# Kernel optimization log

Measured on AMD Instinct MI355X. Metric: run time of the kernel, lower is better.

The kernel has to match this reference:

```python
import jax, jax.numpy as jnp
import numpy as np

N_NODES = 50000
N_EDGES = 800000
N_FEAT = 512
N_HID = 256
N_LAYER = 4
N_CLASS = 40


def setup_inputs() -> dict:
    key = jax.random.key(0)
    ks = jax.random.split(key, 16)
    x = jax.random.normal(ks[0], (N_NODES, N_FEAT), dtype=jnp.float32)
    edge_index = jax.random.randint(ks[1], (2, N_EDGES), 0, N_NODES, dtype=jnp.int64 if jax.config.jax_enable_x64 else jnp.int32)

    def glorot(k, fan_in, fan_out):
        lim = np.sqrt(6.0 / (fan_in + fan_out)).astype(np.float32)
        return jax.random.uniform(k, (fan_in, fan_out), jnp.float32, -lim, lim)

    in_gc_W = glorot(ks[2], N_FEAT, N_HID)
    in_gc_b = jnp.zeros((N_HID,), jnp.float32)
    in_lin_W = glorot(ks[3], N_FEAT, N_HID)
    in_lin_b = jnp.zeros((N_HID,), jnp.float32)
    # n_layer-1 = 3 hidden conv / lin pairs, stacked on leading axis
    convs_W = jnp.stack([glorot(jax.random.fold_in(ks[4], i), N_HID, N_HID) for i in range(N_LAYER - 1)])
    convs_b = jnp.zeros((N_LAYER - 1, N_HID), jnp.float32)
    lins_W = jnp.stack([glorot(jax.random.fold_in(ks[5], i), N_HID, N_HID) for i in range(N_LAYER - 1)])
    lins_b = jnp.zeros((N_LAYER - 1, N_HID), jnp.float32)
    out_W = glorot(ks[6], N_HID * N_LAYER, N_CLASS)
    out_b = jnp.zeros((N_CLASS,), jnp.float32)
    return {
        "x": x, "edge_index": edge_index,
        "in_gc_W": in_gc_W, "in_gc_b": in_gc_b,
        "in_lin_W": in_lin_W, "in_lin_b": in_lin_b,
        "convs_W": convs_W, "convs_b": convs_b,
        "lins_W": lins_W, "lins_b": lins_b,
        "out_W": out_W, "out_b": out_b,
    }


def reference(x, edge_index, in_gc_W, in_gc_b, in_lin_W, in_lin_b,
              convs_W, convs_b, lins_W, lins_b, out_W, out_b):
    src, dst = edge_index[0], edge_index[1]
    n = x.shape[0]
    # GCN symmetric normalization with self-loops: deg = 1 + in-degree
    deg = jnp.zeros((n,), jnp.float32).at[dst].add(1.0) + 1.0
    dinv = jax.lax.rsqrt(deg)
    edge_norm = dinv[src] * dinv[dst]        # [E]
    self_norm = dinv * dinv                  # [N]

    def gcn(h, W, b):
        hw = h @ W                           # [N, out]
        msg = hw[src] * edge_norm[:, None]   # gather + scale
        agg = jax.ops.segment_sum(msg, dst, num_segments=n)
        agg = agg + hw * self_norm[:, None]  # self-loop term
        return agg + b

    # inductive: GCNConv + linear residual; dropout = identity (eval mode)
    h = jax.nn.relu(gcn(x, in_gc_W, in_gc_b) + x @ in_lin_W + in_lin_b)
    xs = [h]
    for i in range(convs_W.shape[0]):
        h = jax.nn.relu(gcn(h, convs_W[i], convs_b[i]) + h @ lins_W[i] + lins_b[i])
        xs.append(h)
    # JumpingKnowledge mode='cat'
    jk = jnp.concatenate(xs, axis=-1)        # [N, n_hid * n_layer]
    return jk @ out_W + out_b
```

## Files before the change

kernel.cpp:

```cpp
#include <hip/hip_runtime.h>

typedef _Float16 half8 __attribute__((ext_vector_type(8)));
typedef _Float16 half4 __attribute__((ext_vector_type(4)));
typedef float floatx4 __attribute__((ext_vector_type(4)));

__device__ __forceinline__ void gld16(const _Float16* g, _Float16* lds_base) {
    __builtin_amdgcn_global_load_lds(
        (const __attribute__((address_space(1))) unsigned int*)g,
        (__attribute__((address_space(3))) unsigned int*)lds_base,
        16, 0, 0);
}

__global__ __launch_bounds__(256) void zero_i32(int* __restrict__ p, int n) {
    int i = blockIdx.x * 256 + threadIdx.x;
    if (i < n) p[i] = 0;
}

__global__ __launch_bounds__(256) void hist_dst(const int* __restrict__ dst,
                                                int* __restrict__ count, int E) {
    int e = blockIdx.x * 256 + threadIdx.x;
    if (e < E) atomicAdd(&count[dst[e]], 1);
}

__global__ __launch_bounds__(256) void cast_f32_f16(const float* __restrict__ in,
                                                    _Float16* __restrict__ out, int n4) {
    int i = blockIdx.x * 256 + threadIdx.x;
    if (i < n4) {
        float4 v = *(const float4*)&in[(size_t)i * 4];
        half4 h = { (_Float16)v.x, (_Float16)v.y, (_Float16)v.z, (_Float16)v.w };
        *(half4*)&out[(size_t)i * 4] = h;
    }
}

__global__ __launch_bounds__(256) void transpose_cast_tiled(
    const float* __restrict__ W, _Float16* __restrict__ WT, int K, int N)
{
    __shared__ _Float16 t[32][33];
    const int k0 = blockIdx.x * 32, n0 = blockIdx.y * 32;
    const int tx = threadIdx.x & 31, ty = threadIdx.x >> 5;
    #pragma unroll
    for (int i = 0; i < 4; ++i) {
        int k = k0 + ty + i * 8, n = n0 + tx;
        float v = (k < K && n < N) ? W[(size_t)k * N + n] : 0.0f;
        t[ty + i * 8][tx] = (_Float16)v;
    }
    __syncthreads();
    #pragma unroll
    for (int i = 0; i < 4; ++i) {
        int n = n0 + ty + i * 8, k = k0 + tx;
        if (n < N && k < K) WT[(size_t)n * K + k] = t[tx][ty + i * 8];
    }
}

__global__ __launch_bounds__(256) void scan_block(const int* __restrict__ count,
                                                  int* __restrict__ incl,
                                                  int* __restrict__ blocksum,
                                                  float* __restrict__ dinv, int n) {
    __shared__ int tmp[256];
    int t = threadIdx.x;
    int i = blockIdx.x * 256 + t;
    int v = (i < n) ? count[i] : 0;
    if (i < n) dinv[i] = rsqrtf(1.0f + (float)v);
    tmp[t] = v;
    __syncthreads();
    for (int off = 1; off < 256; off <<= 1) {
        int x = (t >= off) ? tmp[t - off] : 0;
        __syncthreads();
        tmp[t] += x;
        __syncthreads();
    }
    if (i < n) incl[i] = tmp[t];
    if (t == 255) blocksum[blockIdx.x] = tmp[255];
}

__global__ __launch_bounds__(256) void scan_top(const int* __restrict__ blocksum,
                                                int* __restrict__ blockoff, int nb) {
    __shared__ int tmp[256];
    int t = threadIdx.x;
    int v = (t < nb) ? blocksum[t] : 0;
    tmp[t] = v;
    __syncthreads();
    for (int off = 1; off < 256; off <<= 1) {
        int x = (t >= off) ? tmp[t - off] : 0;
        __syncthreads();
        tmp[t] += x;
        __syncthreads();
    }
    if (t < nb) blockoff[t] = tmp[t] - v;
}

__global__ __launch_bounds__(256) void make_rowptr(const int* __restrict__ incl,
                                                   const int* __restrict__ count,
                                                   const int* __restrict__ blockoff,
                                                   int* __restrict__ rowptr,
                                                   int* __restrict__ cursor, int n) {
    int i = blockIdx.x * 256 + threadIdx.x;
    if (i < n) {
        int r = incl[i] - count[i] + blockoff[blockIdx.x];
        rowptr[i] = r;
        cursor[i] = r;
    }
}

__global__ __launch_bounds__(256) void scatter_perm(const int* __restrict__ src,
                                                    const int* __restrict__ dst,
                                                    const float* __restrict__ dinv,
                                                    int* __restrict__ cursor,
                                                    int2* __restrict__ sorted_meta, int E) {
    int e = blockIdx.x * 256 + threadIdx.x;
    if (e < E) {
        int d = dst[e], s = src[e];
        int slot = atomicAdd(&cursor[d], 1);
        sorted_meta[slot] = make_int2(s, __float_as_int(dinv[s] * dinv[d]));
    }
}

template<bool DUAL>
__global__ __launch_bounds__(256) void gemm_mfma(
    const _Float16* __restrict__ A, int lda,
    const _Float16* __restrict__ BT, int Nrows,
    const float* __restrict__ bias0, const float* __restrict__ bias1,
    _Float16* __restrict__ lin_h, _Float16* __restrict__ hw,
    float* __restrict__ Cf, int ldc,
    int M, int K)
{
    __shared__ _Float16 As[128 * 64];
    __shared__ _Float16 Bs[128 * 64];

    const int tid  = threadIdx.x;
    const int wave = tid >> 6;
    const int lane = tid & 63;
    const int q    = lane >> 4;
    const int r    = lane & 15;

    const int wm = (wave & 1) * 64;
    const int wn = (wave >> 1) * 64;

    const int bn = blockIdx.x * 128;
    const int bm = blockIdx.y * 128;

    const int srow  = wave * 32;
    const int lrow8 = lane >> 3;
    const int cp    = lane & 7;

    floatx4 acc[4][4] = {};

    for (int k0 = 0; k0 < K; k0 += 64) {
        #pragma unroll
        for (int t = 0; t < 4; ++t) {
            int lrow = srow + t * 8 + lrow8;
            int c    = cp ^ (lrow & 7);
            int gm = bm + lrow; if (gm > M - 1) gm = M - 1;
            gld16(&A[(size_t)gm * lda + k0 + c * 8], &As[(srow + t * 8) * 64]);
            int gn = bn + lrow; if (gn > Nrows - 1) gn = Nrows - 1;
            gld16(&BT[(size_t)gn * K + k0 + c * 8], &Bs[(srow + t * 8) * 64]);
        }
        __syncthreads();

        #pragma unroll
        for (int kk = 0; kk < 2; ++kk) {
            const int sc = ((kk << 2) | q) ^ (r & 7);
            half8 af[4], bf[4];
            #pragma unroll
            for (int mi = 0; mi < 4; ++mi)
                af[mi] = *(const half8*)&As[(wm + mi * 16 + r) * 64 + sc * 8];
            #pragma unroll
            for (int ni = 0; ni < 4; ++ni)
                bf[ni] = *(const half8*)&Bs[(wn + ni * 16 + r) * 64 + sc * 8];
            #pragma unroll
            for (int mi = 0; mi < 4; ++mi)
                #pragma unroll
                for (int ni = 0; ni < 4; ++ni)
                    acc[mi][ni] = __builtin_amdgcn_mfma_f32_16x16x32_f16(
                        af[mi], bf[ni], acc[mi][ni], 0, 0, 0);
        }
        __syncthreads();
    }

    if (DUAL) {
        const bool islin = (bn < 256);
        _Float16* dstp = islin ? lin_h : hw;
        #pragma unroll
        for (int ni = 0; ni < 4; ++ni) {
            int col = bn + wn + ni * 16 + r;
            int c2  = islin ? col : col - 256;
            float badd = islin ? (bias0[col] + bias1[col]) : 0.0f;
            #pragma unroll
            for (int mi = 0; mi < 4; ++mi)
                #pragma unroll
                for (int reg = 0; reg < 4; ++reg) {
                    int gm = bm + wm + mi * 16 + q * 4 + reg;
                    if (gm < M)
                        dstp[(size_t)gm * 256 + c2] = (_Float16)(acc[mi][ni][reg] + badd);
                }
        }
    } else {
        #pragma unroll
        for (int ni = 0; ni < 4; ++ni) {
            int col = bn + wn + ni * 16 + r;
            if (col >= Nrows) continue;
            float badd = bias0 ? bias0[col] : 0.0f;
            #pragma unroll
            for (int mi = 0; mi < 4; ++mi)
                #pragma unroll
                for (int reg = 0; reg < 4; ++reg) {
                    int gm = bm + wm + mi * 16 + q * 4 + reg;
                    if (gm < M)
                        Cf[(size_t)gm * ldc + col] = acc[mi][ni][reg] + badd;
                }
        }
    }
}

__global__ __launch_bounds__(256) void aggregate_csr(
    const int* __restrict__ rowptr, const int* __restrict__ count,
    const int2* __restrict__ sorted_meta,
    const float* __restrict__ dinv,
    const _Float16* __restrict__ hw,
    const _Float16* __restrict__ lin_h,
    _Float16* __restrict__ jk_col, int n)
{
    const int bx    = blockIdx.x;
    const int xslot = bx & 7;
    const int half  = xslot >> 2;
    const int chunk = ((bx >> 3) << 2) + (xslot & 3);
    const int wave  = threadIdx.x >> 6;
    const int lane  = threadIdx.x & 63;
    const int i     = chunk * 4 + wave;
    if (i >= n) return;

    const int qw = lane >> 4;
    const int fl = lane & 15;
    const int fbase = half * 128 + fl * 8;

    const int start = rowptr[i];
    const int deg   = count[i];

    float accf[8] = {};
    if (qw == 0) {
        half8 l8 = *(const half8*)&lin_h[(size_t)i * 256 + fbase];
        #pragma unroll
        for (int t = 0; t < 8; ++t) accf[t] = (float)l8[t];
    } else if (qw == 1) {
        float di = dinv[i];
        float sn = di * di;
        half8 s8 = *(const half8*)&hw[(size_t)i * 256 + fbase];
        #pragma unroll
        for (int t = 0; t < 8; ++t) accf[t] = (float)s8[t] * sn;
    }

    for (int base = 0; base < deg; base += 64) {
        int m = deg - base;
        if (m > 64) m = 64;
        int2 meta = make_int2(0, 0);
        if (lane < m) meta = sorted_meta[start + base + lane];

        for (int j = 0; j < m; j += 16) {
            half8 hv[4];
            float nm[4];
            #pragma unroll
            for (int k2 = 0; k2 < 4; ++k2) {
                int e   = j + k2 * 4 + qw;
                int idx = (e < m) ? e : (m - 1);
                int s   = __shfl(meta.x, idx, 64);
                int nmb = __shfl(meta.y, idx, 64);
                nm[k2]  = (e < m) ? __int_as_float(nmb) : 0.0f;
                hv[k2]  = *(const half8*)&hw[(size_t)s * 256 + fbase];
            }
            #pragma unroll
            for (int k2 = 0; k2 < 4; ++k2)
                #pragma unroll
                for (int t = 0; t < 8; ++t)
                    accf[t] = fmaf((float)hv[k2][t], nm[k2], accf[t]);
        }
    }

    #pragma unroll
    for (int t = 0; t < 8; ++t) {
        accf[t] += __shfl_xor(accf[t], 16, 64);
        accf[t] += __shfl_xor(accf[t], 32, 64);
    }

    if (qw == 0) {
        half8 o;
        #pragma unroll
        for (int t = 0; t < 8; ++t) o[t] = (_Float16)fmaxf(accf[t], 0.0f);
        *(half8*)&jk_col[(size_t)i * 1024 + fbase] = o;
    }
}

extern "C" void kernel_launch(void* const* d_in, const int* in_sizes, int n_in,
                              void* d_out, int out_size, void* d_ws, size_t ws_size,
                              hipStream_t stream) {
    const float* x        = (const float*)d_in[0];
    const int*   ei       = (const int*)d_in[1];
    const float* in_gc_W  = (const float*)d_in[2];
    const float* in_gc_b  = (const float*)d_in[3];
    const float* in_lin_W = (const float*)d_in[4];
    const float* in_lin_b = (const float*)d_in[5];
    const float* convs_W  = (const float*)d_in[6];
    const float* convs_b  = (const float*)d_in[7];
    const float* lins_W   = (const float*)d_in[8];
    const float* lins_b   = (const float*)d_in[9];
    const float* out_W    = (const float*)d_in[10];
    const float* out_b    = (const float*)d_in[11];

    const int N = 50000;
    const int E = in_sizes[1] / 2;
    const int F = 512, H = 256, L = 4, NC = 40;

    const int* src = ei;
    const int* dst = ei + E;

    char* ws = (char*)d_ws;
    auto carve = [&](size_t bytes) { void* p = ws; ws += (bytes + 255) & ~(size_t)255; return p; };
    float*    dinv        = (float*)carve((size_t)N * 4);
    int*      count       = (int*)  carve((size_t)N * 4);
    int*      incl        = (int*)  carve((size_t)N * 4);
    int*      rowptr      = (int*)  carve((size_t)N * 4);
    int*      cursor      = (int*)  carve((size_t)N * 4);
    int*      blocksum    = (int*)  carve(256 * 4);
    int*      blockoff    = (int*)  carve(256 * 4);
    int2*     sorted_meta = (int2*) carve((size_t)E * 8);
    _Float16* xh          = (_Float16*)carve((size_t)N * F * 2);
    _Float16* w0comb      = (_Float16*)carve((size_t)512 * F * 2);
    _Float16* wcomb       = (_Float16*)carve((size_t)3 * 512 * H * 2);
    _Float16* outWT       = (_Float16*)carve((size_t)NC * H * L * 2);
    _Float16* lin_h       = (_Float16*)carve((size_t)N * H * 2);
    _Float16* hw          = (_Float16*)carve((size_t)N * H * 2);
    _Float16* jk_h        = (_Float16*)carve((size_t)N * H * L * 2);
    float*    out         = (float*)d_out;

    const int nbN = (N + 255) / 256;
    const int nbE = (E + 255) / 256;

    zero_i32<<<nbN, 256, 0, stream>>>(count, N);
    hist_dst<<<nbE, 256, 0, stream>>>(dst, count, E);
    scan_block<<<nbN, 256, 0, stream>>>(count, incl, blocksum, dinv, N);
    scan_top<<<1, 256, 0, stream>>>(blocksum, blockoff, nbN);
    make_rowptr<<<nbN, 256, 0, stream>>>(incl, count, blockoff, rowptr, cursor, N);
    scatter_perm<<<nbE, 256, 0, stream>>>(src, dst, dinv, cursor, sorted_meta, E);

    cast_f32_f16<<<(N * F / 4 + 255) / 256, 256, 0, stream>>>(x, xh, N * F / 4);
    {
        dim3 tg((F + 31) / 32, (H + 31) / 32);
        transpose_cast_tiled<<<tg, 256, 0, stream>>>(in_lin_W, w0comb,                F, H);
        transpose_cast_tiled<<<tg, 256, 0, stream>>>(in_gc_W,  w0comb + (size_t)H * F, F, H);
        dim3 th((H + 31) / 32, (H + 31) / 32);
        for (int l = 0; l < 3; ++l) {
            _Float16* wl = wcomb + (size_t)l * 512 * H;
            transpose_cast_tiled<<<th, 256, 0, stream>>>(lins_W  + (size_t)l * H * H, wl,                 H, H);
            transpose_cast_tiled<<<th, 256, 0, stream>>>(convs_W + (size_t)l * H * H, wl + (size_t)H * H, H, H);
        }
        dim3 to((H * L + 31) / 32, (NC + 31) / 32);
        transpose_cast_tiled<<<to, 256, 0, stream>>>(out_W, outWT, H * L, NC);
    }

    const dim3 dgrid(4, (N + 127) / 128);
    const dim3 ogrid(1, (N + 127) / 128);
    const int agg_blocks = 2 * ((N + 3) / 4);

    for (int l = 0; l < L; ++l) {
        const _Float16* Ah = (l == 0) ? xh : (jk_h + (size_t)(l - 1) * H);
        int lda            = (l == 0) ? F : H * L;
        int K              = (l == 0) ? F : H;
        const _Float16* BT = (l == 0) ? w0comb : (wcomb + (size_t)(l - 1) * 512 * H);
        const float* gcB   = (l == 0) ? in_gc_b  : (convs_b + (size_t)(l - 1) * H);
        const float* liB   = (l == 0) ? in_lin_b : (lins_b  + (size_t)(l - 1) * H);

        gemm_mfma<true><<<dgrid, 256, 0, stream>>>(Ah, lda, BT, 512, liB, gcB,
                                                   lin_h, hw, nullptr, 0, N, K);
        aggregate_csr<<<agg_blocks, 256, 0, stream>>>(rowptr, count, sorted_meta,
                                                      dinv, hw, lin_h, jk_h + (size_t)l * H, N);
    }

    gemm_mfma<false><<<ogrid, 256, 0, stream>>>(jk_h, H * L, outWT, NC, out_b, nullptr,
                                                nullptr, nullptr, out, NC, N, H * L);
}
```

Baseline: 725.8 us.

## Fuse setup kernels, remap GEMM grid for XCD locality, specialize output GEMM, simplify aggregation

Folds the count zeroing into a wider 8-element fp32-to-fp16 cast kernel and collapses the eight weight transpose launches into three batched launches. The dual GEMM now uses a 1D grid with a block-index swizzle that groups M tiles across XCD slots. The output projection gets a dedicated 256-row kernel that uses a 64-wide N tile instead of 128. The CSR aggregation drops the shuffle-based metadata broadcast in favour of direct per-lane metadata loads, eight edges deep. Together these cut launch count and wasted output-GEMM work, but the metadata reads are now redundant across lanes and the swizzle may shift L2 behaviour.

Measured after the change: 816.9 us. +12.6%, slower.

```diff
diff --git a/kernel.cpp b/kernel.cpp
--- a/kernel.cpp
+++ b/kernel.cpp
@@ -11,9 +11,18 @@
         16, 0, 0);
 }
 
-__global__ __launch_bounds__(256) void zero_i32(int* __restrict__ p, int n) {
+__global__ __launch_bounds__(256) void cast_x_zero(const float* __restrict__ in,
+                                                   _Float16* __restrict__ out, int n8,
+                                                   int* __restrict__ count, int nzero) {
     int i = blockIdx.x * 256 + threadIdx.x;
-    if (i < n) p[i] = 0;
+    if (i < n8) {
+        float4 v0 = *(const float4*)&in[(size_t)i * 8];
+        float4 v1 = *(const float4*)&in[(size_t)i * 8 + 4];
+        half8 h = { (_Float16)v0.x, (_Float16)v0.y, (_Float16)v0.z, (_Float16)v0.w,
+                    (_Float16)v1.x, (_Float16)v1.y, (_Float16)v1.z, (_Float16)v1.w };
+        *(half8*)&out[(size_t)i * 8] = h;
+    }
+    if (i < nzero) count[i] = 0;
 }
 
 __global__ __launch_bounds__(256) void hist_dst(const int* __restrict__ dst,
@@ -22,22 +31,9 @@
     if (e < E) atomicAdd(&count[dst[e]], 1);
 }
 
-__global__ __launch_bounds__(256) void cast_f32_f16(const float* __restrict__ in,
-                                                    _Float16* __restrict__ out, int n4) {
-    int i = blockIdx.x * 256 + threadIdx.x;
-    if (i < n4) {
-        float4 v = *(const float4*)&in[(size_t)i * 4];
-        half4 h = { (_Float16)v.x, (_Float16)v.y, (_Float16)v.z, (_Float16)v.w };
-        *(half4*)&out[(size_t)i * 4] = h;
-    }
-}
-
-__global__ __launch_bounds__(256) void transpose_cast_tiled(
-    const float* __restrict__ W, _Float16* __restrict__ WT, int K, int N)
-{
+__device__ __forceinline__ void tc_tile(const float* W, _Float16* WT, int K, int N,
+                                        int k0, int n0, int tx, int ty) {
     __shared__ _Float16 t[32][33];
-    const int k0 = blockIdx.x * 32, n0 = blockIdx.y * 32;
-    const int tx = threadIdx.x & 31, ty = threadIdx.x >> 5;
     #pragma unroll
     for (int i = 0; i < 4; ++i) {
         int k = k0 + ty + i * 8, n = n0 + tx;
@@ -50,6 +46,34 @@
         int n = n0 + ty + i * 8, k = k0 + tx;
         if (n < N && k < K) WT[(size_t)n * K + k] = t[tx][ty + i * 8];
     }
+}
+
+__global__ __launch_bounds__(256) void transpose_cast_in(
+    const float* __restrict__ Wl, const float* __restrict__ Wg,
+    _Float16* __restrict__ dst, int K, int N)
+{
+    const float* W = blockIdx.z ? Wg : Wl;
+    _Float16* D = dst + (size_t)blockIdx.z * N * K;
+    tc_tile(W, D, K, N, blockIdx.x * 32, blockIdx.y * 32,
+            threadIdx.x & 31, threadIdx.x >> 5);
+}
+
+__global__ __launch_bounds__(256) void transpose_cast_hid(
+    const float* __restrict__ lins, const float* __restrict__ convs,
+    _Float16* __restrict__ wcomb)
+{
+    const int l = blockIdx.z >> 1, j = blockIdx.z & 1;
+    const float* W = (j ? convs : lins) + (size_t)l * 256 * 256;
+    _Float16* D = wcomb + (size_t)l * 512 * 256 + (size_t)j * 256 * 256;
+    tc_tile(W, D, 256, 256, blockIdx.x * 32, blockIdx.y * 32,
+            threadIdx.x & 31, threadIdx.x >> 5);
+}
+
+__global__ __launch_bounds__(256) void transpose_cast_one(
+    const float* __restrict__ W, _Float16* __restrict__ WT, int K, int N)
+{
+    tc_tile(W, WT, K, N, blockIdx.x * 32, blockIdx.y * 32,
+            threadIdx.x & 31, threadIdx.x >> 5);
 }
 
 __global__ __launch_bounds__(256) void scan_block(const int* __restrict__ count,
@@ -115,33 +139,28 @@
     }
 }
 
-template<bool DUAL>
-__global__ __launch_bounds__(256) void gemm_mfma(
+__global__ __launch_bounds__(256) void gemm_dual(
     const _Float16* __restrict__ A, int lda,
-    const _Float16* __restrict__ BT, int Nrows,
+    const _Float16* __restrict__ BT, int K,
     const float* __restrict__ bias0, const float* __restrict__ bias1,
     _Float16* __restrict__ lin_h, _Float16* __restrict__ hw,
-    float* __restrict__ Cf, int ldc,
-    int M, int K)
-{
+    int M, int m_tiles)
+{
+    const int b     = blockIdx.x;
+    const int x     = b & 7;
+    const int inner = b >> 3;
+    const int n_t   = inner & 3;
+    const int m_t   = (inner >> 2) * 8 + x;
+    if (m_t >= m_tiles) return;
+    const int bm = m_t * 128, bn = n_t * 128;
+
     __shared__ _Float16 As[128 * 64];
     __shared__ _Float16 Bs[128 * 64];
 
-    const int tid  = threadIdx.x;
-    const int wave = tid >> 6;
-    const int lane = tid & 63;
-    const int q    = lane >> 4;
-    const int r    = lane & 15;
-
-    const int wm = (wave & 1) * 64;
-    const int wn = (wave >> 1) * 64;
-
-    const int bn = blockIdx.x * 128;
-    const int bm = blockIdx.y * 128;
-
-    const int srow  = wave * 32;
-    const int lrow8 = lane >> 3;
-    const int cp    = lane & 7;
+    const int wave = threadIdx.x >> 6, lane = threadIdx.x & 63;
+    const int q = lane >> 4, r = lane & 15;
+    const int wm = (wave & 1) * 64, wn = (wave >> 1) * 64;
+    const int srow = wave * 32, lrow8 = lane >> 3, cp = lane & 7;
 
     floatx4 acc[4][4] = {};
 
@@ -152,7 +171,7 @@
             int c    = cp ^ (lrow & 7);
             int gm = bm + lrow; if (gm > M - 1) gm = M - 1;
             gld16(&A[(size_t)gm * lda + k0 + c * 8], &As[(srow + t * 8) * 64]);
-            int gn = bn + lrow; if (gn > Nrows - 1) gn = Nrows - 1;
+            int gn = bn + lrow;
             gld16(&BT[(size_t)gn * K + k0 + c * 8], &Bs[(srow + t * 8) * 64]);
         }
         __syncthreads();
@@ -177,39 +196,101 @@
         __syncthreads();
     }
 
-    if (DUAL) {
-        const bool islin = (bn < 256);
-        _Float16* dstp = islin ? lin_h : hw;
-        #pragma unroll
-        for (int ni = 0; ni < 4; ++ni) {
-            int col = bn + wn + ni * 16 + r;
-            int c2  = islin ? col : col - 256;
-            float badd = islin ? (bias0[col] + bias1[col]) : 0.0f;
+    const bool islin = (bn < 256);
+    _Float16* dstp = islin ? lin_h : hw;
+    const int cbase = (islin ? bn : bn - 256) + wn;
+    float badd[4];
+    #pragma unroll
+    for (int ni = 0; ni < 4; ++ni) {
+        int col = bn + wn + ni * 16 + r;
+        badd[ni] = islin ? (bias0[col] + bias1[col]) : 0.0f;
+    }
+    #pragma unroll
+    for (int mi = 0; mi < 4; ++mi)
+        #pragma unroll
+        for (int reg = 0; reg < 4; ++reg) {
+            int gm = bm + wm + mi * 16 + q * 4 + reg;
+            if (gm >= M) continue;
+            #pragma unroll
+            for (int ni = 0; ni < 4; ++ni)
+                dstp[(size_t)gm * 256 + cbase + ni * 16 + r] =
+                    (_Float16)(acc[mi][ni][reg] + badd[ni]);
+        }
+}
+
+__global__ __launch_bounds__(256) void gemm_out(
+    const _Float16* __restrict__ A,
+    const _Float16* __restrict__ BT,
+    const float* __restrict__ bias,
+    float* __restrict__ Cf, int M)
+{
+    const int bm = blockIdx.x * 256;
+    __shared__ _Float16 As[256 * 64];
+    __shared__ _Float16 Bs[64 * 64];
+
+    const int wave = threadIdx.x >> 6, lane = threadIdx.x & 63;
+    const int q = lane >> 4, r = lane & 15;
+    const int wm = wave * 64;
+    const int lrow8 = lane >> 3, cp = lane & 7;
+
+    floatx4 acc[4][4] = {};
+
+    for (int k0 = 0; k0 < 1024; k0 += 64) {
+        #pragma unroll
+        for (int t = 0; t < 8; ++t) {
+            int lrow = wm + t * 8 + lrow8;
+            int c    = cp ^ (lrow & 7);
+            int gm = bm + lrow; if (gm > M - 1) gm = M - 1;
+            gld16(&A[(size_t)gm * 1024 + k0 + c * 8], &As[(wm + t * 8) * 64]);
+        }
+        #pragma unroll
+        for (int t = 0; t < 2; ++t) {
+            int brow = wave * 16 + t * 8 + lrow8;
+            int c    = cp ^ (brow & 7);
+            int gn = brow; if (gn > 39) gn = 39;
+            gld16(&BT[(size_t)gn * 1024 + k0 + c * 8], &Bs[(wave * 16 + t * 8) * 64]);
+        }
+        __syncthreads();
+
+        #pragma unroll
+        for (int kk = 0; kk < 2; ++kk) {
+            const int sc = ((kk << 2) | q) ^ (r & 7);
+            half8 af[4], bf[4];
+            #pragma unroll
+            for (int mi = 0; mi < 4; ++mi)
+                af[mi] = *(const half8*)&As[(wm + mi * 16 + r) * 64 + sc * 8];
+            #pragma unroll
+            for (int ni = 0; ni < 4; ++ni)
+                bf[ni] = *(const half8*)&Bs[(ni * 16 + r) * 64 + sc * 8];
             #pragma unroll
             for (int mi = 0; mi < 4; ++mi)
                 #pragma unroll
-                for (int reg = 0; reg < 4; ++reg) {
-                    int gm = bm + wm + mi * 16 + q * 4 + reg;
-                    if (gm < M)
-                        dstp[(size_t)gm * 256 + c2] = (_Float16)(acc[mi][ni][reg] + badd);
-                }
-        }
-    } else {
-        #pragma unroll
-        for (int ni = 0; ni < 4; ++ni) {
-            int col = bn + wn + ni * 16 + r;
-            if (col >= Nrows) continue;
-            float badd = bias0 ? bias0[col] : 0.0f;
-            #pragma unroll
-            for (int mi = 0; mi < 4; ++mi)
-                #pragma unroll
-                for (int reg = 0; reg < 4; ++reg) {
-                    int gm = bm + wm + mi * 16 + q * 4 + reg;
-                    if (gm < M)
-                        Cf[(size_t)gm * ldc + col] = acc[mi][ni][reg] + badd;
-                }
-        }
-    }
+                for (int ni = 0; ni < 4; ++ni)
+                    acc[mi][ni] = __builtin_amdgcn_mfma_f32_16x16x32_f16(
+                        af[mi], bf[ni], acc[mi][ni], 0, 0, 0);
+        }
+        __syncthreads();
+    }
+
+    float badd[4];
+    #pragma unroll
+    for (int ni = 0; ni < 4; ++ni) {
+        int col = ni * 16 + r;
+        badd[ni] = (col < 40) ? bias[col] : 0.0f;
+    }
+    #pragma unroll
+    for (int mi = 0; mi < 4; ++mi)
+        #pragma unroll
+        for (int reg = 0; reg < 4; ++reg) {
+            int gm = bm + wm + mi * 16 + q * 4 + reg;
+            if (gm >= M) continue;
+            #pragma unroll
+            for (int ni = 0; ni < 4; ++ni) {
+                int col = ni * 16 + r;
+                if (col < 40)
+                    Cf[(size_t)gm * 40 + col] = acc[mi][ni][reg] + badd[ni];
+            }
+        }
 }
 
 __global__ __launch_bounds__(256) void aggregate_csr(
@@ -249,30 +330,23 @@
         for (int t = 0; t < 8; ++t) accf[t] = (float)s8[t] * sn;
     }
 
-    for (int base = 0; base < deg; base += 64) {
-        int m = deg - base;
-        if (m > 64) m = 64;
-        int2 meta = make_int2(0, 0);
-        if (lane < m) meta = sorted_meta[start + base + lane];
-
-        for (int j = 0; j < m; j += 16) {
-            half8 hv[4];
-            float nm[4];
-            #pragma unroll
-            for (int k2 = 0; k2 < 4; ++k2) {
-                int e   = j + k2 * 4 + qw;
-                int idx = (e < m) ? e : (m - 1);
-                int s   = __shfl(meta.x, idx, 64);
-                int nmb = __shfl(meta.y, idx, 64);
-                nm[k2]  = (e < m) ? __int_as_float(nmb) : 0.0f;
-                hv[k2]  = *(const half8*)&hw[(size_t)s * 256 + fbase];
-            }
-            #pragma unroll
-            for (int k2 = 0; k2 < 4; ++k2)
-                #pragma unroll
-                for (int t = 0; t < 8; ++t)
-                    accf[t] = fmaf((float)hv[k2][t], nm[k2], accf[t]);
-        }
+    const int2* mp = sorted_meta + start;
+    for (int j = 0; j < deg; j += 32) {
+        half8 hv[8];
+        float nm[8];
+        #pragma unroll
+        for (int k2 = 0; k2 < 8; ++k2) {
+            int e  = j + k2 * 4 + qw;
+            int ec = (e < deg) ? e : (deg - 1);
+            int2 mt = mp[ec];
+            nm[k2] = (e < deg) ? __int_as_float(mt.y) : 0.0f;
+            hv[k2] = *(const half8*)&hw[(size_t)mt.x * 256 + fbase];
+        }
+        #pragma unroll
+        for (int k2 = 0; k2 < 8; ++k2)
+            #pragma unroll
+            for (int t = 0; t < 8; ++t)
+                accf[t] = fmaf((float)hv[k2][t], nm[k2], accf[t]);
     }
 
     #pragma unroll
@@ -334,31 +408,21 @@
     const int nbN = (N + 255) / 256;
     const int nbE = (E + 255) / 256;
 
-    zero_i32<<<nbN, 256, 0, stream>>>(count, N);
+    cast_x_zero<<<(N * F / 8 + 255) / 256, 256, 0, stream>>>(x, xh, N * F / 8, count, N);
     hist_dst<<<nbE, 256, 0, stream>>>(dst, count, E);
     scan_block<<<nbN, 256, 0, stream>>>(count, incl, blocksum, dinv, N);
     scan_top<<<1, 256, 0, stream>>>(blocksum, blockoff, nbN);
     make_rowptr<<<nbN, 256, 0, stream>>>(incl, count, blockoff, rowptr, cursor, N);
     scatter_perm<<<nbE, 256, 0, stream>>>(src, dst, dinv, cursor, sorted_meta, E);
 
-    cast_f32_f16<<<(N * F / 4 + 255) / 256, 256, 0, stream>>>(x, xh, N * F / 4);
-    {
-        dim3 tg((F + 31) / 32, (H + 31) / 32);
-        transpose_cast_tiled<<<tg, 256, 0, stream>>>(in_lin_W, w0comb,                F, H);
-        transpose_cast_tiled<<<tg, 256, 0, stream>>>(in_gc_W,  w0comb + (size_t)H * F, F, H);
-        dim3 th((H + 31) / 32, (H + 31) / 32);
-        for (int l = 0; l < 3; ++l) {
-            _Float16* wl = wcomb + (size_t)l * 512 * H;
-            transpose_cast_tiled<<<th, 256, 0, stream>>>(lins_W  + (size_t)l * H * H, wl,                 H, H);
-            transpose_cast_tiled<<<th, 256, 0, stream>>>(convs_W + (size_t)l * H * H, wl + (size_t)H * H, H, H);
-        }
-        dim3 to((H * L + 31) / 32, (NC + 31) / 32);
-        transpose_cast_tiled<<<to, 256, 0, stream>>>(out_W, outWT, H * L, NC);
-    }
-
-    const dim3 dgrid(4, (N + 127) / 128);
-    const dim3 ogrid(1, (N + 127) / 128);
-    const int agg_blocks = 2 * ((N + 3) / 4);
+    transpose_cast_in<<<dim3(F / 32, H / 32, 2), 256, 0, stream>>>(in_lin_W, in_gc_W, w0comb, F, H);
+    transpose_cast_hid<<<dim3(H / 32, H / 32, 6), 256, 0, stream>>>(lins_W, convs_W, wcomb);
+    transpose_cast_one<<<dim3(H * L / 32, (NC + 31) / 32), 256, 0, stream>>>(out_W, outWT, H * L, NC);
+
+    const int m_tiles = (N + 127) / 128;
+    const int dual_blocks = 8 * ((m_tiles + 7) / 8) * 4;
+    const int agg_blocks  = 2 * ((N + 3) / 4);
+    const int out_blocks  = (N + 255) / 256;
 
     for (int l = 0; l < L; ++l) {
         const _Float16* Ah = (l == 0) ? xh : (jk_h + (size_t)(l - 1) * H);
@@ -368,12 +432,11 @@
         const float* gcB   = (l == 0) ? in_gc_b  : (convs_b + (size_t)(l - 1) * H);
         const float* liB   = (l == 0) ? in_lin_b : (lins_b  + (size_t)(l - 1) * H);
 
-        gemm_mfma<true><<<dgrid, 256, 0, stream>>>(Ah, lda, BT, 512, liB, gcB,
-                                                   lin_h, hw, nullptr, 0, N, K);
+        gemm_dual<<<dual_blocks, 256, 0, stream>>>(Ah, lda, BT, K, liB, gcB,
+                                                   lin_h, hw, N, m_tiles);
         aggregate_csr<<<agg_blocks, 256, 0, stream>>>(rowptr, count, sorted_meta,
                                                       dinv, hw, lin_h, jk_h + (size_t)l * H, N);
     }
 
-    gemm_mfma<false><<<ogrid, 256, 0, stream>>>(jk_h, H * L, outWT, NC, out_b, nullptr,
-                                                nullptr, nullptr, out, NC, N, H * L);
-}
+    gemm_out<<<out_blocks, 256, 0, stream>>>(jk_h, outWT, out_b, out, N);
+}
```
